# Kernel tuning notes

Measured on AMD Instinct MI355X. Metric: run time of the kernel, lower is better.

The kernel has to match this reference:

```python
import jax, jax.numpy as jnp
import numpy as np

D_MODEL = 1024
HIDDEN = 4096
NUM_EXPERTS = 8
TOP_K = 2
N_TOKENS = 4 * 2048  # batch * seq


def setup_inputs() -> dict:
    key = jax.random.key(0)
    k_x, k_w, k_i, k1, k2, k3 = jax.random.split(key, 6)
    x = jax.random.normal(k_x, (4, 2048, D_MODEL), dtype=jnp.float32)
    expert_weights = jax.random.uniform(k_w, (N_TOKENS, TOP_K), dtype=jnp.float32)
    expert_indices = jax.random.randint(k_i, (N_TOKENS, TOP_K), 0, NUM_EXPERTS)
    scale = 1.0 / np.sqrt(D_MODEL)
    w1 = jax.random.normal(k1, (NUM_EXPERTS, D_MODEL, HIDDEN), dtype=jnp.float32) * scale
    w3 = jax.random.normal(k3, (NUM_EXPERTS, D_MODEL, HIDDEN), dtype=jnp.float32) * scale
    w2 = jax.random.normal(k2, (NUM_EXPERTS, HIDDEN, D_MODEL), dtype=jnp.float32) * (1.0 / np.sqrt(HIDDEN))
    return {"x": x, "expert_weights": expert_weights, "expert_indices": expert_indices,
            "w1": w1, "w2": w2, "w3": w3}


def reference(x, expert_weights, expert_indices, w1, w2, w3):
    # forward_once of ParallelDroplessMLP (single-rank dropless MoE).
    in_shape = x.shape
    d_model = x.shape[-1]
    num_experts = w1.shape[0]
    xf = x.reshape(-1, d_model)                        # (N, d)
    top_k = expert_weights.shape[-1]
    ew = expert_weights.reshape(-1)                    # (N*top_k,)
    ei = expert_indices.reshape(-1).astype(jnp.int32)  # (N*top_k,)

    # indices_and_bins: stable sort by expert id + histogram
    order = jnp.argsort(ei)                            # (T,) permuted row -> flat (token, k) slot
    tokens_per_expert = jnp.bincount(ei, length=num_experts).astype(jnp.int32)

    # gather: replicate each token top_k times, grouped by expert
    token_of_row = order // top_k                      # (T,)
    xg = jnp.take(xf, token_of_row, axis=0)            # (T, d)

    # grouped GEMM (MegaBlocks-style) SwiGLU per expert via ragged_dot
    h = jax.nn.silu(jax.lax.ragged_dot(xg, w1, tokens_per_expert)) \
        * jax.lax.ragged_dot(xg, w3, tokens_per_expert)            # (T, hidden)
    y = jax.lax.ragged_dot(h, w2, tokens_per_expert)               # (T, d)

    # scatter: weighted un-permute back to token positions
    y = y * ew[order][:, None]
    out = jnp.zeros_like(xf).at[token_of_row].add(y)
    return out.reshape(in_shape), tokens_per_expert
```

## Files before the change

### kernel.cpp

```cpp
#include <hip/hip_runtime.h>

#define NTOK 8192
#define TROWS 16384
#define DM 1024
#define HID 4096
#define NEXP 8
#define MAXT256 72
#define MAXT128 136

typedef __bf16 bf16x8 __attribute__((ext_vector_type(8)));
typedef float  f32x4  __attribute__((ext_vector_type(4)));
typedef short  s16x4  __attribute__((ext_vector_type(4)));
typedef short  s16x8  __attribute__((ext_vector_type(8)));

#define BAR() do { asm volatile("" ::: "memory"); __builtin_amdgcn_s_barrier(); asm volatile("" ::: "memory"); } while(0)
#define VM6() asm volatile("s_waitcnt vmcnt(6)" ::: "memory")
#define VM0() asm volatile("s_waitcnt vmcnt(0)" ::: "memory")

__device__ __forceinline__ short f2bf(float f) {
  union { float f; unsigned u; } v; v.f = f;
  unsigned r = (v.u + 0x7fffu + ((v.u >> 16) & 1u)) >> 16;
  return (short)r;
}
__device__ __forceinline__ float bf2f(short s) {
  union { unsigned u; float f; } z; z.u = ((unsigned)(unsigned short)s) << 16; return z.f;
}

__device__ __forceinline__ void gload16(const short* g, short* l) {
  __builtin_amdgcn_global_load_lds(
      (const __attribute__((address_space(1))) void*)g,
      (__attribute__((address_space(3))) void*)l, 16, 0, 0);
}


__global__ void k_histo(const int* __restrict__ ei, int* __restrict__ meta) {
  int t = blockIdx.x * 256 + threadIdx.x;
  __shared__ int c[NEXP];
  if (threadIdx.x < NEXP) c[threadIdx.x] = 0;
  __syncthreads();
  atomicAdd(&c[ei[t]], 1);
  __syncthreads();
  if (threadIdx.x < NEXP) atomicAdd(&meta[threadIdx.x], c[threadIdx.x]);
}

__global__ void k_plan(int* __restrict__ meta, float* __restrict__ outCounts) {
  if (threadIdx.x != 0 || blockIdx.x != 0) return;
  int off = 0, s = 0, s2 = 0;
  for (int e = 0; e < NEXP; ++e) {
    int ce = meta[e];
    meta[8 + e] = off;
    meta[16 + e] = off;
    outCounts[e] = (float)ce;
    for (int r0 = 0; r0 < ce; r0 += 256) {
      meta[32 + 3*s] = e; meta[32 + 3*s + 1] = off + r0;
      meta[32 + 3*s + 2] = (ce - r0 < 256) ? (ce - r0) : 256; ++s;
    }
    for (int r0 = 0; r0 < ce; r0 += 128) {
      meta[256 + 3*s2] = e; meta[256 + 3*s2 + 1] = off + r0;
      meta[256 + 3*s2 + 2] = (ce - r0 < 128) ? (ce - r0) : 128; ++s2;
    }
    off += ce;
  }
  for (; s < MAXT256; ++s)  { meta[32 + 3*s] = 0;  meta[32 + 3*s + 1] = 0;  meta[32 + 3*s + 2] = 0; }
  for (; s2 < MAXT128; ++s2){ meta[256 + 3*s2] = 0; meta[256 + 3*s2 + 1] = 0; meta[256 + 3*s2 + 2] = 0; }
}

__global__ void k_scatter(const int* __restrict__ ei, int* __restrict__ meta,
                          int* __restrict__ rowmap, int* __restrict__ inv) {
  int t = blockIdx.x * blockDim.x + threadIdx.x;
  if (t < TROWS) {
    int e = ei[t];
    int p = atomicAdd(&meta[16 + e], 1);
    rowmap[p] = t;
    inv[t] = p;
  }
}

__global__ void k_prep(const float* __restrict__ w1, const float* __restrict__ w3,
                       const float* __restrict__ w2, const float* __restrict__ x,
                       short* __restrict__ w1t, short* __restrict__ w3t,
                       short* __restrict__ w2t, short* __restrict__ xb) {
  int b = blockIdx.x;
  int which = b >> 13;
  if (which == 3) {
    int i = (b - 24576) * 256 + threadIdx.x;
    f32x4 v = ((const f32x4*)x)[i];
    s16x4 s = { f2bf(v.x), f2bf(v.y), f2bf(v.z), f2bf(v.w) };
    ((s16x4*)xb)[i] = s;
    return;
  }
  __shared__ float lt[64][65];
  int r = b & 8191;
  const float* in; short* out; int R, C;
  if (which == 0)      { in = w1; out = w1t; R = DM;  C = HID; }
  else if (which == 1) { in = w3; out = w3t; R = DM;  C = HID; }
  else                 { in = w2; out = w2t; R = HID; C = DM;  }
  int nx = C >> 6;
  int e = r >> 10;
  int rem = r & 1023;
  int c0 = (rem & (nx - 1)) * 64, r0 = (rem / nx) * 64;

  int t = threadIdx.x;
  int rr = t >> 4, cc = (t & 15) * 4;
  const float* src = in + ((size_t)e * R + r0 + rr) * C + c0 + cc;
#pragma unroll
  for (int i = 0; i < 4; ++i)
    *(f32x4*)&lt[rr + i*16][cc] = *(const f32x4*)(src + (size_t)i * 16 * C);
  __syncthreads();
  int cN = t >> 4, r4 = (t & 15) * 4;
  short* dst = out + ((size_t)e * C + c0 + cN) * R + r0 + r4;
#pragma unroll
  for (int i = 0; i < 4; ++i) {
    s16x4 o;
#pragma unroll
    for (int j = 0; j < 4; ++j) o[j] = f2bf(lt[r4 + j][cN + i*16]);
    *(s16x4*)(dst + (size_t)i * 16 * R) = o;
  }
}

__global__ __launch_bounds__(512, 2) void k_gemm1(
    const short* __restrict__ xb, const short* __restrict__ w1t, const short* __restrict__ w3t,
    const int* __restrict__ rowmap, const int* __restrict__ meta, short* __restrict__ hbuf) {
  int bid = blockIdx.x;
  int swz = (bid & 7) * 288 + (bid >> 3);
  int slot = swz % MAXT256;
  int bn   = swz / MAXT256;
  int rows = meta[32 + 3*slot + 2];
  if (rows <= 0) return;
  int e    = meta[32 + 3*slot];
  int row0 = meta[32 + 3*slot + 1];

  __shared__ short lA [2][256 * 64];
  __shared__ short lB1[2][128 * 64];
  __shared__ short lB3[2][128 * 64];

  int tid = threadIdx.x, l = tid & 63, w = tid >> 6;
  int wr = (w >> 2) * 128, wc = (w & 3) * 32;
  int lr = l & 15, cb = (l >> 4) * 16, axor = (lr & 7) << 4;
  int srow = l >> 3;
  int scol = ((l & 7) ^ srow) * 8;

  const short* aG[2][2];
#pragma unroll
  for (int h = 0; h < 2; ++h)
#pragma unroll
    for (int i = 0; i < 2; ++i) {
      int r = h*128 + w*16 + i*8 + srow;
      int rc = r < rows ? r : rows - 1;
      int tok = rowmap[row0 + rc] >> 1;
      aG[h][i] = xb + (size_t)tok * DM + scol;
    }
  const short *b1G[2], *b3G[2];
#pragma unroll
  for (int i = 0; i < 2; ++i) {
    size_t grow = (size_t)e * HID + (size_t)bn * 128 + w*16 + i*8 + srow;
    b1G[i] = w1t + grow * DM + scol;
    b3G[i] = w3t + grow * DM + scol;
  }

  f32x4 acc1[2][4][2], acc3[2][4][2];
#pragma unroll
  for (int h = 0; h < 2; ++h)
#pragma unroll
    for (int i = 0; i < 4; ++i)
#pragma unroll
      for (int j = 0; j < 2; ++j) {
        acc1[h][i][j] = (f32x4){0.f,0.f,0.f,0.f};
        acc3[h][i][j] = (f32x4){0.f,0.f,0.f,0.f};
      }

  auto stgA = [&](int buf, int h, int kt) {
    gload16(aG[h][0] + kt, &lA[buf][(h*128 + w*16    ) * 64]);
    gload16(aG[h][1] + kt, &lA[buf][(h*128 + w*16 + 8) * 64]);
  };
  auto stgB1 = [&](int buf, int kt) {
    gload16(b1G[0] + kt, &lB1[buf][(w*16    ) * 64]);
    gload16(b1G[1] + kt, &lB1[buf][(w*16 + 8) * 64]);
  };
  auto stgB3 = [&](int buf, int kt) {
    gload16(b3G[0] + kt, &lB3[buf][(w*16    ) * 64]);
    gload16(b3G[1] + kt, &lB3[buf][(w*16 + 8) * 64]);
  };

  stgA(0, 0, 0); stgA(0, 1, 0); stgB1(0, 0); stgB3(0, 0);
  stgB1(1, 64); stgB3(1, 64); stgA(1, 0, 64);
  VM6();
  BAR();

  const int NT = DM / 64;
  int c = 0;
  for (int t = 0; t < NT; ++t, c ^= 1) {
    int kn  = t*64 + 64;
    int kn2 = t*64 + 128;
    const char* cA  = (const char*)&lA [c][0];
    const char* cB1 = (const char*)&lB1[c][0];
    const char* cB3 = (const char*)&lB3[c][0];

    bf16x8 alo[4][2], b1w[2][2];
#pragma unroll
    for (int i = 0; i < 4; ++i)
#pragma unroll
      for (int kk = 0; kk < 2; ++kk)
        alo[i][kk] = *(const bf16x8*)(cA + (wr + i*16 + lr)*128 + ((kk*64 + cb) ^ axor));
#pragma unroll
    for (int j = 0; j < 2; ++j)
#pragma unroll
      for (int kk = 0; kk < 2; ++kk)
        b1w[j][kk] = *(const bf16x8*)(cB1 + (wc + j*16 + lr)*128 + ((kk*64 + cb) ^ axor));
    if (t + 1 < NT) stgA(c ^ 1, 1, kn);
    BAR();
    __builtin_amdgcn_s_setprio(1);
#pragma unroll
    for (int i = 0; i < 4; ++i)
#pragma unroll
      for (int j = 0; j < 2; ++j)
#pragma unroll
        for (int kk = 0; kk < 2; ++kk)
          acc1[0][i][j] = __builtin_amdgcn_mfma_f32_16x16x32_bf16(alo[i][kk], b1w[j][kk], acc1[0][i][j], 0, 0, 0);
    __builtin_amdgcn_s_setprio(0);
    BAR();

    bf16x8 b3w[2][2];
#pragma unroll
    for (int j = 0; j < 2; ++j)
#pragma unroll
      for (int kk = 0; kk < 2; ++kk)
        b3w[j][kk] = *(const bf16x8*)(cB3 + (wc + j*16 + lr)*128 + ((kk*64 + cb) ^ axor));
    if (t + 2 < NT) stgB1(c, kn2);
    BAR();
    __builtin_amdgcn_s_setprio(1);
#pragma unroll
    for (int i = 0; i < 4; ++i)
#pragma unroll
      for (int j = 0; j < 2; ++j)
#pragma unroll
        for (int kk = 0; kk < 2; ++kk)
          acc3[0][i][j] = __builtin_amdgcn_mfma_f32_16x16x32_bf16(alo[i][kk], b3w[j][kk], acc3[0][i][j], 0, 0, 0);
    __builtin_amdgcn_s_setprio(0);
    BAR();

    bf16x8 ahi[4][2];
#pragma unroll
    for (int i = 0; i < 4; ++i)
#pragma unroll
      for (int kk = 0; kk < 2; ++kk)
        ahi[i][kk] = *(const bf16x8*)(cA + (wr + 64 + i*16 + lr)*128 + ((kk*64 + cb) ^ axor));
    if (t + 2 < NT) stgB3(c, kn2);
    BAR();
    __builtin_amdgcn_s_setprio(1);
#pragma unroll
    for (int i = 0; i < 4; ++i)
#pragma unroll
      for (int j = 0; j < 2; ++j)
#pragma unroll
        for (int kk = 0; kk < 2; ++kk)
          acc1[1][i][j] = __builtin_amdgcn_mfma_f32_16x16x32_bf16(ahi[i][kk], b1w[j][kk], acc1[1][i][j], 0, 0, 0);
    __builtin_amdgcn_s_setprio(0);
    BAR();

    if (t + 2 < NT) stgA(c, 0, kn2);
    __builtin_amdgcn_s_setprio(1);
#pragma unroll
    for (int i = 0; i < 4; ++i)
#pragma unroll
      for (int j = 0; j < 2; ++j)
#pragma unroll
        for (int kk = 0; kk < 2; ++kk)
          acc3[1][i][j] = __builtin_amdgcn_mfma_f32_16x16x32_bf16(ahi[i][kk], b3w[j][kk], acc3[1][i][j], 0, 0, 0);
    __builtin_amdgcn_s_setprio(0);
    if (t < NT - 2) { VM6(); } else { VM0(); }
    BAR();
  }

#pragma unroll
  for (int h = 0; h < 2; ++h)
#pragma unroll
    for (int i = 0; i < 4; ++i)
#pragma unroll
      for (int q = 0; q < 4; ++q) {
        int r = wr + h*64 + i*16 + (l >> 4)*4 + q;
        if (r < rows) {
          size_t base = (size_t)(row0 + r) * HID + (size_t)bn * 128 + wc;
#pragma unroll
          for (int j = 0; j < 2; ++j) {
            float g = acc1[h][i][j][q], u3 = acc3[h][i][j][q];
            float sv = g / (1.f + __expf(-g));
            hbuf[base + j*16 + lr] = f2bf(sv * u3);
          }
        }
      }
}

__global__ __launch_bounds__(256) void k_gemm2(
    const short* __restrict__ hbuf, const short* __restrict__ w2t,
    const int* __restrict__ meta, short* __restrict__ y) {
  int bid = blockIdx.x;
  int xcd = bid & 7, rk = bid >> 3;
  int slot = xcd * 17 + (rk >> 3);
  int bn   = rk & 7;
  int rows = meta[256 + 3*slot + 2];
  if (rows <= 0) return;
  int e    = meta[256 + 3*slot];
  int row0 = meta[256 + 3*slot + 1];

  __shared__ short lA[128 * 64];
  __shared__ short lB[128 * 64];

  int tid = threadIdx.x;
  int l = tid & 63, w = tid >> 6;

  int srow = w*8 + (l >> 3);
  int scol = ((l & 7) ^ (l >> 3)) * 8;

  const short* aG[4];
  for (int p = 0; p < 4; ++p) {
    int r = p*32 + srow;
    int rc = r < rows ? r : rows - 1;
    aG[p] = hbuf + (size_t)(row0 + rc) * HID + scol;
  }
  const short* bG[4];
  for (int p = 0; p < 4; ++p) {
    size_t grow = (size_t)e * DM + (size_t)bn * 128 + p*32 + srow;
    bG[p] = w2t + grow * HID + scol;
  }

  f32x4 acc[4][4];
  for (int i = 0; i < 4; ++i)
    for (int j = 0; j < 4; ++j) acc[i][j] = (f32x4){0.f, 0.f, 0.f, 0.f};

  int wr = (w >> 1) * 64, wc = (w & 1) * 64;
  int lr = l & 15;
  int cb = (l >> 4) * 16;
  int axor = (lr & 7) << 4;

  for (int kt = 0; kt < HID; kt += 64) {
#pragma unroll
    for (int p = 0; p < 4; ++p) {
      gload16(aG[p] + kt, &lA[(p*32 + w*8) * 64]);
      gload16(bG[p] + kt, &lB[(p*32 + w*8) * 64]);
    }
    __syncthreads();
#pragma unroll
    for (int kk2 = 0; kk2 < 2; ++kk2) {
      int co = (kk2*64 + cb) ^ axor;
      bf16x8 a[4], b[4];
#pragma unroll
      for (int i = 0; i < 4; ++i) a[i] = *(const bf16x8*)((const char*)lA + (wr + i*16 + lr)*128 + co);
#pragma unroll
      for (int j = 0; j < 4; ++j) b[j] = *(const bf16x8*)((const char*)lB + (wc + j*16 + lr)*128 + co);
#pragma unroll
      for (int i = 0; i < 4; ++i)
#pragma unroll
        for (int j = 0; j < 4; ++j)
          acc[i][j] = __builtin_amdgcn_mfma_f32_16x16x32_bf16(a[i], b[j], acc[i][j], 0, 0, 0);
    }
    __syncthreads();
  }

  for (int i = 0; i < 4; ++i)
    for (int q = 0; q < 4; ++q) {
      int r = wr + i*16 + (l >> 4)*4 + q;
      if (r < rows) {
        size_t obase = (size_t)(row0 + r) * DM + (size_t)bn * 128 + wc;
        for (int j = 0; j < 4; ++j)
          y[obase + j*16 + lr] = f2bf(acc[i][j][q]);
      }
    }
}

__global__ void k_unperm(const short* __restrict__ y, const int* __restrict__ inv,
                         const float* __restrict__ ew, float* __restrict__ out) {
  int i = blockIdx.x * 256 + threadIdx.x;
  int tok = i >> 7, c = i & 127;
  int p0 = inv[2*tok], p1 = inv[2*tok + 1];
  float w0 = ew[2*tok], w1v = ew[2*tok + 1];
  s16x8 a = ((const s16x8*)y)[(size_t)p0 * 128 + c];
  s16x8 b = ((const s16x8*)y)[(size_t)p1 * 128 + c];
  f32x4 r0, r1;
#pragma unroll
  for (int j = 0; j < 4; ++j) r0[j] = w0 * bf2f(a[j])     + w1v * bf2f(b[j]);
#pragma unroll
  for (int j = 0; j < 4; ++j) r1[j] = w0 * bf2f(a[j + 4]) + w1v * bf2f(b[j + 4]);
  ((f32x4*)out)[2*i]     = r0;
  ((f32x4*)out)[2*i + 1] = r1;
}

extern "C" void kernel_launch(void* const* d_in, const int* in_sizes, int n_in,
                              void* d_out, int out_size, void* d_ws, size_t ws_size,
                              hipStream_t stream) {
  const float* x  = (const float*)d_in[0];
  const float* ew = (const float*)d_in[1];
  const int*   ei = (const int*)d_in[2];
  const float* w1 = (const float*)d_in[3];
  const float* w2 = (const float*)d_in[4];
  const float* w3 = (const float*)d_in[5];
  float* out = (float*)d_out;
  char*  ws  = (char*)d_ws;

  short* w1t = (short*)(ws + 0);
  short* w3t = (short*)(ws + 67108864);
  short* w2t = (short*)(ws + 134217728);
  short* xb  = (short*)(ws + 201326592);
  short* hb  = (short*)(ws + 218103808);
  int*   meta   = (int*)(ws + 352321536);
  int*   rowmap = (int*)(ws + 352321536 + 8192);
  int*   inv    = (int*)(ws + 352321536 + 73728);
  short* y      = (short*)(ws + 0);

  hipMemsetAsync(meta, 0, NEXP * sizeof(int), stream);
  k_histo<<<TROWS / 256, 256, 0, stream>>>(ei, meta);
  k_plan<<<1, 64, 0, stream>>>(meta, out + (size_t)NTOK * DM);
  k_scatter<<<TROWS / 256, 256, 0, stream>>>(ei, meta, rowmap, inv);
  k_prep<<<32768, 256, 0, stream>>>(w1, w3, w2, x, w1t, w3t, w2t, xb);
  k_gemm1<<<MAXT256 * (HID/128), 512, 0, stream>>>(xb, w1t, w3t, rowmap, meta, hb);
  k_gemm2<<<MAXT128 * (DM/128), 256, 0, stream>>>(hb, w2t, meta, y);
  k_unperm<<<NTOK * DM / 8 / 256, 256, 0, stream>>>(y, inv, ew, out);
}
```

Before: 712.0 us.

## Merge gate/up MFMA phases in gemm1 and parallelize plan kernel across experts

The gemm1 main loop drops from four barrier-separated MFMA phases to two. B1 and B3 fragments are loaded together and the acc1/acc3 MFMAs are interleaved, which removes two barriers per K-step and gives the scheduler longer MFMA runs. The cost is higher register pressure from holding b3w alongside b1w, and a changed overlap between the staging loads and compute. Separately, k_plan now computes each expert's offsets and tile lists in parallel, one thread per expert, instead of a single serial thread.

```diff
diff --git a/kernel.cpp b/kernel.cpp
--- a/kernel.cpp
+++ b/kernel.cpp
@@ -44,10 +44,24 @@
 }
 
 __global__ void k_plan(int* __restrict__ meta, float* __restrict__ outCounts) {
-  if (threadIdx.x != 0 || blockIdx.x != 0) return;
-  int off = 0, s = 0, s2 = 0;
-  for (int e = 0; e < NEXP; ++e) {
-    int ce = meta[e];
+  int tid = threadIdx.x;
+  int cnts[NEXP];
+#pragma unroll
+  for (int j = 0; j < NEXP; ++j) cnts[j] = meta[j];
+  int tot256 = 0, tot128 = 0;
+#pragma unroll
+  for (int j = 0; j < NEXP; ++j) {
+    tot256 += (cnts[j] + 255) >> 8;
+    tot128 += (cnts[j] + 127) >> 7;
+  }
+  if (tid < NEXP) {
+    int e = tid, off = 0, s = 0, s2 = 0;
+    for (int j = 0; j < e; ++j) {
+      off += cnts[j];
+      s   += (cnts[j] + 255) >> 8;
+      s2  += (cnts[j] + 127) >> 7;
+    }
+    int ce = cnts[e];
     meta[8 + e] = off;
     meta[16 + e] = off;
     outCounts[e] = (float)ce;
@@ -59,10 +73,13 @@
       meta[256 + 3*s2] = e; meta[256 + 3*s2 + 1] = off + r0;
       meta[256 + 3*s2 + 2] = (ce - r0 < 128) ? (ce - r0) : 128; ++s2;
     }
-    off += ce;
-  }
-  for (; s < MAXT256; ++s)  { meta[32 + 3*s] = 0;  meta[32 + 3*s + 1] = 0;  meta[32 + 3*s + 2] = 0; }
-  for (; s2 < MAXT128; ++s2){ meta[256 + 3*s2] = 0; meta[256 + 3*s2 + 1] = 0; meta[256 + 3*s2 + 2] = 0; }
+  }
+  for (int s = tot256 + tid; s < MAXT256; s += 256) {
+    meta[32 + 3*s] = 0; meta[32 + 3*s + 1] = 0; meta[32 + 3*s + 2] = 0;
+  }
+  for (int s2 = tot128 + tid; s2 < MAXT128; s2 += 256) {
+    meta[256 + 3*s2] = 0; meta[256 + 3*s2 + 1] = 0; meta[256 + 3*s2 + 2] = 0;
+  }
 }
 
 __global__ void k_scatter(const int* __restrict__ ei, int* __restrict__ meta,
@@ -196,7 +213,7 @@
     const char* cB1 = (const char*)&lB1[c][0];
     const char* cB3 = (const char*)&lB3[c][0];
 
-    bf16x8 alo[4][2], b1w[2][2];
+    bf16x8 alo[4][2], b1w[2][2], b3w[2][2];
 #pragma unroll
     for (int i = 0; i < 4; ++i)
 #pragma unroll
@@ -205,8 +222,10 @@
 #pragma unroll
     for (int j = 0; j < 2; ++j)
 #pragma unroll
-      for (int kk = 0; kk < 2; ++kk)
+      for (int kk = 0; kk < 2; ++kk) {
         b1w[j][kk] = *(const bf16x8*)(cB1 + (wc + j*16 + lr)*128 + ((kk*64 + cb) ^ axor));
+        b3w[j][kk] = *(const bf16x8*)(cB3 + (wc + j*16 + lr)*128 + ((kk*64 + cb) ^ axor));
+      }
     if (t + 1 < NT) stgA(c ^ 1, 1, kn);
     BAR();
     __builtin_amdgcn_s_setprio(1);
@@ -215,28 +234,12 @@
 #pragma unroll
       for (int j = 0; j < 2; ++j)
 #pragma unroll
-        for (int kk = 0; kk < 2; ++kk)
+        for (int kk = 0; kk < 2; ++kk) {
           acc1[0][i][j] = __builtin_amdgcn_mfma_f32_16x16x32_bf16(alo[i][kk], b1w[j][kk], acc1[0][i][j], 0, 0, 0);
+          acc3[0][i][j] = __builtin_amdgcn_mfma_f32_16x16x32_bf16(alo[i][kk], b3w[j][kk], acc3[0][i][j], 0, 0, 0);
+        }
     __builtin_amdgcn_s_setprio(0);
-    BAR();
-
-    bf16x8 b3w[2][2];
-#pragma unroll
-    for (int j = 0; j < 2; ++j)
-#pragma unroll
-      for (int kk = 0; kk < 2; ++kk)
-        b3w[j][kk] = *(const bf16x8*)(cB3 + (wc + j*16 + lr)*128 + ((kk*64 + cb) ^ axor));
     if (t + 2 < NT) stgB1(c, kn2);
-    BAR();
-    __builtin_amdgcn_s_setprio(1);
-#pragma unroll
-    for (int i = 0; i < 4; ++i)
-#pragma unroll
-      for (int j = 0; j < 2; ++j)
-#pragma unroll
-        for (int kk = 0; kk < 2; ++kk)
-          acc3[0][i][j] = __builtin_amdgcn_mfma_f32_16x16x32_bf16(alo[i][kk], b3w[j][kk], acc3[0][i][j], 0, 0, 0);
-    __builtin_amdgcn_s_setprio(0);
     BAR();
 
     bf16x8 ahi[4][2];
@@ -253,21 +256,12 @@
 #pragma unroll
       for (int j = 0; j < 2; ++j)
 #pragma unroll
-        for (int kk = 0; kk < 2; ++kk)
+        for (int kk = 0; kk < 2; ++kk) {
           acc1[1][i][j] = __builtin_amdgcn_mfma_f32_16x16x32_bf16(ahi[i][kk], b1w[j][kk], acc1[1][i][j], 0, 0, 0);
+          acc3[1][i][j] = __builtin_amdgcn_mfma_f32_16x16x32_bf16(ahi[i][kk], b3w[j][kk], acc3[1][i][j], 0, 0, 0);
+        }
     __builtin_amdgcn_s_setprio(0);
-    BAR();
-
     if (t + 2 < NT) stgA(c, 0, kn2);
-    __builtin_amdgcn_s_setprio(1);
-#pragma unroll
-    for (int i = 0; i < 4; ++i)
-#pragma unroll
-      for (int j = 0; j < 2; ++j)
-#pragma unroll
-        for (int kk = 0; kk < 2; ++kk)
-          acc3[1][i][j] = __builtin_amdgcn_mfma_f32_16x16x32_bf16(ahi[i][kk], b3w[j][kk], acc3[1][i][j], 0, 0, 0);
-    __builtin_amdgcn_s_setprio(0);
     if (t < NT - 2) { VM6(); } else { VM0(); }
     BAR();
   }
@@ -409,7 +403,7 @@
 
   hipMemsetAsync(meta, 0, NEXP * sizeof(int), stream);
   k_histo<<<TROWS / 256, 256, 0, stream>>>(ei, meta);
-  k_plan<<<1, 64, 0, stream>>>(meta, out + (size_t)NTOK * DM);
+  k_plan<<<1, 256, 0, stream>>>(meta, out + (size_t)NTOK * DM);
   k_scatter<<<TROWS / 256, 256, 0, stream>>>(ei, meta, rowmap, inv);
   k_prep<<<32768, 256, 0, stream>>>(w1, w3, w2, x, w1t, w3t, w2t, xb);
   k_gemm1<<<MAXT256 * (HID/128), 512, 0, stream>>>(xb, w1t, w3t, rowmap, meta, hb);
```

After: 723.3 us. Within noise of the previous version (+1.6%).
